# Performance work log

Measured on AMD Instinct MI355X. Metric: run time of the kernel, lower is better.

## Reference

```python
import jax, jax.numpy as jnp
import numpy as np

# Static config (from module defaults)
B, L, D, DR, R, P, PH, F = 4, 2048, 512, 256, 3, 5, 3, 1536
MAX_BANKS = 7  # S4Intelligence zero-pads unused bank slots
EPS = 1e-5


def _ln(x, s, b):
    m = x.mean(-1, keepdims=True)
    v = x.var(-1, keepdims=True)
    return (x - m) / jnp.sqrt(v + EPS) * s + b


def setup_inputs() -> dict:
    key = jax.random.key(0)
    ks = iter(jax.random.split(key, 40))
    r = lambda *s: jax.random.normal(next(ks), s, jnp.float32) * 0.02
    return dict(
        x=jax.random.normal(next(ks), (B, L, D), jnp.float32),
        reg_init=r(R, DR),
        ffn_ln_s=jnp.ones((PH, D)), ffn_ln_b=jnp.zeros((PH, D)),
        ffn_w1=r(PH, D, F), ffn_b1=jnp.zeros((PH, F)),
        ffn_w2=r(PH, F, D), ffn_b2=jnp.zeros((PH, D)),
        gate_w=r(P, PH, R * DR + D, D), gate_b=jnp.zeros((P, PH, D)),
        wproj_w=r(P, PH, R, D, DR),
        wgate_w=r(P, PH, R, D), wgate_b=jnp.zeros((P, PH, R)),
        s4_q=r(MAX_BANKS * R * DR, D), s4_k=r(D, D), s4_v=r(D, D),
        s4_sum=r(D, R * DR), s4_ln_s=jnp.ones(D), s4_ln_b=jnp.zeros(D),
        ms3_w=r(P * R * DR, P), ms3_b=jnp.zeros(P),
        m4_q=r(P * R * DR, D), m4_k=r(D, D), m4_v=r(D, D), m4_out=r(D, D),
        m4_ln_s=jnp.ones(D), m4_ln_b=jnp.zeros(D),
        out_ln_s=jnp.ones(D), out_ln_b=jnp.zeros(D),
    )


def _forward(x, reg_init, ffn_ln_s, ffn_ln_b, ffn_w1, ffn_b1, ffn_w2, ffn_b2,
             gate_w, gate_b, wproj_w, wgate_w, wgate_b,
             s4_q, s4_k, s4_v, s4_sum, s4_ln_s, s4_ln_b,
             ms3_w, ms3_b, m4_q, m4_k, m4_v, m4_out, m4_ln_s, m4_ln_b,
             out_ln_s, out_ln_b):
    scale = D ** -0.5

    # MetaS3: per-pass contribution gates from (initial) register banks
    ms3_in = jnp.tile(reg_init.reshape(-1), P)          # [P*R*DR]
    pass_w = jax.nn.sigmoid(ms3_in @ ms3_w + ms3_b)      # [P]

    def s4_read(banks, residual):
        # S4Intelligence: single-global-query attention over residual,
        # query from flattened register banks zero-padded to MAX_BANKS slots.
        flat = [bk.reshape(-1) for bk in banks]
        used = R * DR * len(banks)
        pad = MAX_BANKS * R * DR - used
        parts = flat + ([jnp.zeros((pad,), x.dtype)] if pad > 0 else [])
        q = jnp.concatenate(parts) @ s4_q                # [D]
        xn = _ln(residual, s4_ln_s, s4_ln_b)
        k = xn @ s4_k
        v = xn @ s4_v
        a = jax.nn.softmax(jnp.einsum('d,bld->bl', q, k) * scale, axis=-1)
        summ = jnp.einsum('bl,bld->bd', a, v).mean(0)    # [D]
        return (summ @ s4_sum).reshape(R, DR)            # register updates

    residual = x
    banks = []
    for p in range(P):  # 5 level-passes: L0^, L1^, L2, L1v, L0v
        regs = reg_init + s4_read(banks, residual)       # [R, DR]
        for ph in range(PH):  # prep / converge / consolidate
            xn = _ln(residual, ffn_ln_s[ph], ffn_ln_b[ph])
            delta = jax.nn.gelu(xn @ ffn_w1[ph] + ffn_b1[ph],
                                approximate=False) @ ffn_w2[ph] + ffn_b2[ph]
            # S3LevelControl.gate_phase
            summary = delta.mean((0, 1))                 # [D]
            gin = jnp.concatenate([regs.reshape(-1), summary])
            gate = jax.nn.sigmoid(gin @ gate_w[p, ph] + gate_b[p, ph])  # [D]
            residual = residual + pass_w[p] * (gate * delta)
            wg = jax.nn.sigmoid(jnp.einsum('d,rd->r', summary, wgate_w[p, ph])
                                + wgate_b[p, ph])        # [R]
            upd = jnp.einsum('d,rdk->rk', summary, wproj_w[p, ph])  # [R, DR]
            regs = regs + wg[:, None] * upd
        banks.append(regs)

    # MetaS4: final intelligence scan over all refined banks
    q = jnp.concatenate([bk.reshape(-1) for bk in banks]) @ m4_q  # [D]
    xn = _ln(residual, m4_ln_s, m4_ln_b)
    k = xn @ m4_k
    v = xn @ m4_v
    a = jax.nn.softmax(jnp.einsum('d,bld->bl', q, k) * scale, axis=-1)
    summ = jnp.einsum('bl,bld->bd', a, v)                # [B, D]
    residual = residual + (summ @ m4_out)[:, None, :]
    return _ln(residual, out_ln_s, out_ln_b)


def reference(x, reg_init, ffn_ln_s, ffn_ln_b, ffn_w1, ffn_b1, ffn_w2, ffn_b2,
              gate_w, gate_b, wproj_w, wgate_w, wgate_b,
              s4_q, s4_k, s4_v, s4_sum, s4_ln_s, s4_ln_b,
              ms3_w, ms3_b, m4_q, m4_k, m4_v, m4_out, m4_ln_s, m4_ln_b,
              out_ln_s, out_ln_b):
    return _forward(x, reg_init, ffn_ln_s, ffn_ln_b, ffn_w1, ffn_b1, ffn_w2,
                    ffn_b2, gate_w, gate_b, wproj_w, wgate_w, wgate_b,
                    s4_q, s4_k, s4_v, s4_sum, s4_ln_s, s4_ln_b,
                    ms3_w, ms3_b, m4_q, m4_k, m4_v, m4_out, m4_ln_s, m4_ln_b,
                    out_ln_s, out_ln_b)
```

## Files before the change

kernel.cpp:

```cpp
#include <hip/hip_runtime.h>
#include <stdint.h>

typedef __bf16 bf16;
typedef __bf16 bf16x8 __attribute__((ext_vector_type(8)));
typedef float floatx4 __attribute__((ext_vector_type(4)));

#define EPS 1e-5f

__device__ __forceinline__ float wave_red_sum(float v) {
#pragma unroll
  for (int off = 32; off; off >>= 1) v += __shfl_xor(v, off, 64);
  return v;
}
__device__ __forceinline__ float wave_red_max(float v) {
#pragma unroll
  for (int off = 32; off; off >>= 1) v = fmaxf(v, __shfl_xor(v, off, 64));
  return v;
}
__device__ __forceinline__ float sigmoidf(float x) { return 1.f / (1.f + expf(-x)); }

__device__ __forceinline__ void gload_lds16(const bf16* g, bf16* l) {
  __builtin_amdgcn_global_load_lds(
      (const __attribute__((address_space(1))) char*)(g),
      (__attribute__((address_space(3))) char*)(l), 16, 0, 0);
}

__global__ __launch_bounds__(256) void transpose_cast_kernel(
    const float* __restrict__ in, bf16* __restrict__ out, int R, int C) {
  __shared__ float tile[32][33];
  const size_t boff = (size_t)blockIdx.z * R * C;
  in += boff; out += boff;
  int tx = threadIdx.x, ty = threadIdx.y;
  int c0 = blockIdx.x * 32, r0 = blockIdx.y * 32;
#pragma unroll
  for (int j = 0; j < 32; j += 8)
    tile[ty + j][tx] = in[(size_t)(r0 + ty + j) * C + c0 + tx];
  __syncthreads();
#pragma unroll
  for (int j = 0; j < 32; j += 8)
    out[(size_t)(c0 + ty + j) * R + r0 + tx] = (bf16)tile[tx][ty + j];
}

template <int BM, int BN, int WM, int WN, int MODE>
__global__ __launch_bounds__(256) void gemm_kernel(
    const bf16* __restrict__ A, const bf16* __restrict__ Bt,
    const float* __restrict__ bias, bf16* __restrict__ outb,
    float* __restrict__ gsum, int N, int K) {
  constexpr int MI = WM / 16, NI = WN / 16, NWC = BN / WN;
  __shared__ bf16 As[BM * 64];
  __shared__ bf16 Bs[BN * 64];
  const int tid = threadIdx.x, l = tid & 63, w = tid >> 6;
  const int wr = w / NWC, wc = w % NWC;
  const int m0 = blockIdx.x * BM, n0 = blockIdx.y * BN;
  const int lrow8 = l >> 3;
  const int lcol8 = (((l & 7) ^ lrow8) * 8);
  const int quad = l >> 4, lane16 = l & 15;
  const int r7 = lane16 & 7;

  floatx4 acc[MI][NI];
#pragma unroll
  for (int mi = 0; mi < MI; ++mi)
#pragma unroll
    for (int ni = 0; ni < NI; ++ni) acc[mi][ni] = (floatx4){0.f, 0.f, 0.f, 0.f};

  const bf16* gA = A + (size_t)m0 * K;
  const bf16* gB = Bt + (size_t)n0 * K;

  for (int k0 = 0; k0 < K; k0 += 64) {
#pragma unroll
    for (int i = 0; i < BM / 32; ++i) {
      int rb = w * (BM / 4) + i * 8;
      gload_lds16(gA + (size_t)(rb + lrow8) * K + k0 + lcol8, As + rb * 64);
    }
#pragma unroll
    for (int i = 0; i < BN / 32; ++i) {
      int rb = w * (BN / 4) + i * 8;
      gload_lds16(gB + (size_t)(rb + lrow8) * K + k0 + lcol8, Bs + rb * 64);
    }
    __syncthreads();
#pragma unroll
    for (int kk = 0; kk < 64; kk += 32) {
      const int g = (kk >> 3) + quad;
      bf16x8 af[MI], bfv[NI];
#pragma unroll
      for (int mi = 0; mi < MI; ++mi) {
        int r = wr * WM + mi * 16 + lane16;
        af[mi] = *(const bf16x8*)(As + r * 64 + ((g ^ r7) * 8));
      }
#pragma unroll
      for (int ni = 0; ni < NI; ++ni) {
        int r = wc * WN + ni * 16 + lane16;
        bfv[ni] = *(const bf16x8*)(Bs + r * 64 + ((g ^ r7) * 8));
      }
#pragma unroll
      for (int mi = 0; mi < MI; ++mi)
#pragma unroll
        for (int ni = 0; ni < NI; ++ni)
          acc[mi][ni] = __builtin_amdgcn_mfma_f32_16x16x32_bf16(af[mi], bfv[ni], acc[mi][ni], 0, 0, 0);
    }
    __syncthreads();
  }

  float psum[NI];
#pragma unroll
  for (int ni = 0; ni < NI; ++ni) psum[ni] = 0.f;

#pragma unroll
  for (int ni = 0; ni < NI; ++ni) {
    const int gn = n0 + wc * WN + ni * 16 + lane16;
    const float bv = bias[gn];
#pragma unroll
    for (int mi = 0; mi < MI; ++mi) {
#pragma unroll
      for (int i = 0; i < 4; ++i) {
        const int gm = m0 + wr * WM + mi * 16 + quad * 4 + i;
        float v = acc[mi][ni][i] + bv;
        if constexpr (MODE == 0) {
          float ge = 0.5f * v * (1.f + erff(v * 0.7071067811865475f));
          outb[(size_t)gm * N + gn] = (bf16)ge;
        } else {
          outb[(size_t)gm * N + gn] = (bf16)v;
          psum[ni] += v;
        }
      }
    }
  }
  if constexpr (MODE == 1) {
    float* cs = (float*)As;
    __syncthreads();
    for (int t = tid; t < BN; t += 256) cs[t] = 0.f;
    __syncthreads();
#pragma unroll
    for (int ni = 0; ni < NI; ++ni)
      atomicAdd(&cs[wc * WN + ni * 16 + lane16], psum[ni]);
    __syncthreads();
    for (int t = tid; t < BN; t += 256) atomicAdd(&gsum[n0 + t], cs[t]);
  }
}

__global__ __launch_bounds__(256) void gemv_kernel(
    const float* __restrict__ vin, int vstride, const float* __restrict__ M,
    size_t mstride, int K, int N, float alpha, float* __restrict__ outp,
    int ostride) {
  const int l = threadIdx.x & 63, wv = threadIdx.x >> 6;
  const int col = blockIdx.x * 64 + l;
  const int KS = gridDim.y;
  const int Kc = (K + KS - 1) / KS;
  const int k0 = blockIdx.y * Kc;
  const int k1 = min(K, k0 + Kc);
  const float* v = vin + (size_t)blockIdx.z * vstride;
  const float* Mp = M + (size_t)blockIdx.z * mstride;
  float acc = 0.f;
  for (int k = k0 + wv; k < k1; k += 4)
    acc += v[k] * Mp[(size_t)k * N + col];
  __shared__ float sh[4][64];
  sh[wv][l] = acc;
  __syncthreads();
  if (wv == 0) {
    float r = (sh[0][l] + sh[1][l] + sh[2][l] + sh[3][l]) * alpha;
    atomicAdd(&outp[(size_t)blockIdx.z * ostride + col], r);
  }
}

__global__ __launch_bounds__(256) void small_gemvs_kernel(
    const float* __restrict__ regs, const float* __restrict__ summary,
    const float* __restrict__ gwp, const float* __restrict__ gbp,
    const float* __restrict__ wpp, float* __restrict__ gate_pre,
    float* __restrict__ ubuf) {
  const int z = blockIdx.z;
  const float* v;
  const float* M;
  float* outp;
  int K, N;
  float alpha;
  if (z == 0)      { v = regs;    M = gwp;             outp = gate_pre; K = 768; N = 512; alpha = 1.f; }
  else if (z == 1) { v = summary; M = gwp + 768 * 512; outp = gate_pre; K = 512; N = 512; alpha = 1.f / 8192.f; }
  else { int r = z - 2; v = summary; M = wpp + (size_t)r * 512 * 256; outp = ubuf + r * 256; K = 512; N = 256; alpha = 1.f / 8192.f; }
  const int l = threadIdx.x & 63, wv = threadIdx.x >> 6;
  const int col = blockIdx.x * 64 + l;
  if (blockIdx.x * 64 >= N) return;
  const int Kc = K / 8;
  const int k0 = blockIdx.y * Kc, k1 = k0 + Kc;
  float acc = 0.f;
  for (int k = k0 + wv; k < k1; k += 4)
    acc += v[k] * M[(size_t)k * N + col];
  __shared__ float sh[4][64];
  sh[wv][l] = acc;
  __syncthreads();
  if (wv == 0) {
    float r = (sh[0][l] + sh[1][l] + sh[2][l] + sh[3][l]) * alpha;
    if (z == 0 && blockIdx.y == 0) r += gbp[col];
    atomicAdd(&outp[col], r);
  }
}

__global__ __launch_bounds__(256) void init3_kernel(
    float* __restrict__ a, int na, float* __restrict__ b, int nb,
    float* __restrict__ c, const float* __restrict__ csrc, int nc) {
  const int t = blockIdx.x * 256 + threadIdx.x;
  if (t < na) a[t] = 0.f;
  if (t < nb) b[t] = 0.f;
  if (t < nc) c[t] = csrc ? csrc[t] : 0.f;
}

__global__ __launch_bounds__(256) void ln_cast_kernel(
    const float* __restrict__ res, const float* __restrict__ s,
    const float* __restrict__ b, bf16* __restrict__ xn,
    float* __restrict__ summary, float* __restrict__ gp0,
    float* __restrict__ gp1, float* __restrict__ ubuf) {
  if (blockIdx.x == 0) {
    const int t = threadIdx.x;
    summary[t] = 0.f; summary[t + 256] = 0.f;
    gp0[t] = 0.f; gp0[t + 256] = 0.f;
    gp1[t] = 0.f; gp1[t + 256] = 0.f;
    ubuf[t] = 0.f; ubuf[t + 256] = 0.f; ubuf[t + 512] = 0.f;
  }
  const int wid = threadIdx.x >> 6, l = threadIdx.x & 63;
  const int row = blockIdx.x * 4 + wid;
  const int cb = l * 8;
  const float* x = res + (size_t)row * 512 + cb;
  float4 a0 = *(const float4*)x, a1 = *(const float4*)(x + 4);
  float v[8] = {a0.x, a0.y, a0.z, a0.w, a1.x, a1.y, a1.z, a1.w};
  float sum = 0.f, sq = 0.f;
#pragma unroll
  for (int j = 0; j < 8; ++j) { sum += v[j]; sq += v[j] * v[j]; }
  sum = wave_red_sum(sum); sq = wave_red_sum(sq);
  float m = sum * (1.f / 512.f);
  float rstd = rsqrtf(sq * (1.f / 512.f) - m * m + EPS);
  bf16x8 o;
#pragma unroll
  for (int j = 0; j < 8; ++j) o[j] = (bf16)((v[j] - m) * rstd * s[cb + j] + b[cb + j]);
  *(bf16x8*)(xn + (size_t)row * 512 + cb) = o;
}

__global__ __launch_bounds__(256) void resid_ln_kernel(
    float* __restrict__ res, const bf16* __restrict__ delta,
    const float* __restrict__ gp, const float* __restrict__ passw, int p,
    const float* __restrict__ s, const float* __restrict__ b,
    bf16* __restrict__ xn) {
  const int wid = threadIdx.x >> 6, l = threadIdx.x & 63;
  const int row = blockIdx.x * 4 + wid;
  const int cb = l * 8;
  const float pw = passw[p];
  float* x = res + (size_t)row * 512 + cb;
  float4 a0 = *(const float4*)x, a1 = *(const float4*)(x + 4);
  bf16x8 dv = *(const bf16x8*)(delta + (size_t)row * 512 + cb);
  float4 g0 = *(const float4*)(gp + cb), g1 = *(const float4*)(gp + cb + 4);
  float gg[8] = {g0.x, g0.y, g0.z, g0.w, g1.x, g1.y, g1.z, g1.w};
  float v[8] = {a0.x, a0.y, a0.z, a0.w, a1.x, a1.y, a1.z, a1.w};
#pragma unroll
  for (int j = 0; j < 8; ++j) v[j] += pw * sigmoidf(gg[j]) * (float)dv[j];
  *(float4*)x = make_float4(v[0], v[1], v[2], v[3]);
  *(float4*)(x + 4) = make_float4(v[4], v[5], v[6], v[7]);
  float sum = 0.f, sq = 0.f;
#pragma unroll
  for (int j = 0; j < 8; ++j) { sum += v[j]; sq += v[j] * v[j]; }
  sum = wave_red_sum(sum); sq = wave_red_sum(sq);
  float m = sum * (1.f / 512.f);
  float rstd = rsqrtf(sq * (1.f / 512.f) - m * m + EPS);
  bf16x8 o;
#pragma unroll
  for (int j = 0; j < 8; ++j) o[j] = (bf16)((v[j] - m) * rstd * s[cb + j] + b[cb + j]);
  *(bf16x8*)(xn + (size_t)row * 512 + cb) = o;
}

__global__ __launch_bounds__(256) void attn_logits_kernel(
    const float* __restrict__ res, const float* __restrict__ s,
    const float* __restrict__ b, const float* __restrict__ kq,
    float* __restrict__ logits, float* __restrict__ czero) {
  if (blockIdx.x == 0) {
#pragma unroll
    for (int j = 0; j < 8; ++j) czero[threadIdx.x * 8 + j] = 0.f;
  }
  const int wid = threadIdx.x >> 6, l = threadIdx.x & 63;
  const int row = blockIdx.x * 4 + wid;
  const int cb = l * 8;
  const float* x = res + (size_t)row * 512 + cb;
  float4 a0 = *(const float4*)x, a1 = *(const float4*)(x + 4);
  float v[8] = {a0.x, a0.y, a0.z, a0.w, a1.x, a1.y, a1.z, a1.w};
  float sum = 0.f, sq = 0.f;
#pragma unroll
  for (int j = 0; j < 8; ++j) { sum += v[j]; sq += v[j] * v[j]; }
  sum = wave_red_sum(sum); sq = wave_red_sum(sq);
  float m = sum * (1.f / 512.f);
  float rstd = rsqrtf(sq * (1.f / 512.f) - m * m + EPS);
  float dot = 0.f;
#pragma unroll
  for (int j = 0; j < 8; ++j)
    dot += ((v[j] - m) * rstd * s[cb + j] + b[cb + j]) * kq[cb + j];
  dot = wave_red_sum(dot);
  if (l == 0) logits[row] = dot;
}

__global__ __launch_bounds__(256) void softmax_kernel(float* __restrict__ attn) {
  __shared__ float red[4];
  const int t = threadIdx.x;
  float* p = attn + blockIdx.x * 2048;
  float v[8];
#pragma unroll
  for (int j = 0; j < 8; ++j) v[j] = p[t * 8 + j];
  float mx = v[0];
#pragma unroll
  for (int j = 1; j < 8; ++j) mx = fmaxf(mx, v[j]);
  mx = wave_red_max(mx);
  if ((t & 63) == 0) red[t >> 6] = mx;
  __syncthreads();
  mx = fmaxf(fmaxf(red[0], red[1]), fmaxf(red[2], red[3]));
  __syncthreads();
  float s = 0.f;
#pragma unroll
  for (int j = 0; j < 8; ++j) { v[j] = expf(v[j] - mx); s += v[j]; }
  s = wave_red_sum(s);
  if ((t & 63) == 0) red[t >> 6] = s;
  __syncthreads();
  float inv = 1.f / (red[0] + red[1] + red[2] + red[3]);
#pragma unroll
  for (int j = 0; j < 8; ++j) p[t * 8 + j] = v[j] * inv;
}

__global__ __launch_bounds__(256) void wsum_kernel(
    const float* __restrict__ res, const float* __restrict__ s,
    const float* __restrict__ b, const float* __restrict__ attn,
    float* __restrict__ cout, int per_batch) {
  __shared__ float csh[512];
  const int tid = threadIdx.x, l = tid & 63, wv = tid >> 6;
  for (int t = tid; t < 512; t += 256) csh[t] = 0.f;
  __syncthreads();
  const int cb = l * 8;
  float sl[8], bl[8];
#pragma unroll
  for (int j = 0; j < 8; ++j) { sl[j] = s[cb + j]; bl[j] = b[cb + j]; }
  float pf[8] = {};
  const int base_row = blockIdx.x * 32;
  for (int rr = wv; rr < 32; rr += 4) {
    int row = base_row + rr;
    const float* x = res + (size_t)row * 512 + cb;
    float4 a0 = *(const float4*)x, a1 = *(const float4*)(x + 4);
    float v[8] = {a0.x, a0.y, a0.z, a0.w, a1.x, a1.y, a1.z, a1.w};
    float sum = 0.f, sq = 0.f;
#pragma unroll
    for (int j = 0; j < 8; ++j) { sum += v[j]; sq += v[j] * v[j]; }
    sum = wave_red_sum(sum); sq = wave_red_sum(sq);
    float m = sum * (1.f / 512.f);
    float rstd = rsqrtf(sq * (1.f / 512.f) - m * m + EPS);
    float aw = attn ? attn[row] : (1.f / 2048.f);
#pragma unroll
    for (int j = 0; j < 8; ++j) pf[j] += aw * ((v[j] - m) * rstd * sl[j] + bl[j]);
  }
#pragma unroll
  for (int j = 0; j < 8; ++j) atomicAdd(&csh[cb + j], pf[j]);
  __syncthreads();
  float* outp = cout + (per_batch ? (blockIdx.x >> 6) * 512 : 0);
  for (int t = tid; t < 512; t += 256) atomicAdd(&outp[t], csh[t]);
}

__global__ __launch_bounds__(256) void kq_kernel(
    const float* __restrict__ KM, const float* __restrict__ q, float scale,
    float* __restrict__ kq) {
  const int d = blockIdx.x * 4 + (threadIdx.x >> 6), l = threadIdx.x & 63;
  float a = 0.f;
  for (int j = l; j < 512; j += 64) a += KM[(size_t)d * 512 + j] * q[j];
  a = wave_red_sum(a);
  if (l == 0) kq[d] = a * scale;
}

__global__ __launch_bounds__(256) void reg_final_kernel(
    const float* __restrict__ regsA, float* __restrict__ ubuf,
    float* __restrict__ summary, const float* __restrict__ wgw,
    const float* __restrict__ wgb, float* __restrict__ regsB,
    float* __restrict__ gp_next) {
  __shared__ float wg[3];
  const int l = threadIdx.x & 63, wv = threadIdx.x >> 6;
  if (wv < 3) {
    float sg = 0.f;
    for (int d = l; d < 512; d += 64) sg += summary[d] * wgw[wv * 512 + d];
    sg = wave_red_sum(sg) * (1.f / 8192.f);
    if (l == 0) wg[wv] = sigmoidf(sg + wgb[wv]);
  }
  __syncthreads();
  for (int j = threadIdx.x; j < 768; j += 256)
    regsB[j] = regsA[j] + wg[j >> 8] * ubuf[j];
  __syncthreads();
  const int t = threadIdx.x;
  summary[t] = 0.f; summary[t + 256] = 0.f;
  gp_next[t] = 0.f; gp_next[t + 256] = 0.f;
  ubuf[t] = 0.f; ubuf[t + 256] = 0.f; ubuf[t + 512] = 0.f;
}

__global__ __launch_bounds__(64) void passw_kernel(
    const float* __restrict__ reg_init, const float* __restrict__ ms3_w,
    const float* __restrict__ ms3_b, float* __restrict__ pass_w) {
  const int l = threadIdx.x;
  float acc[5] = {};
  for (int i = l; i < 3840; i += 64) {
    float v = reg_init[i % 768];
#pragma unroll
    for (int p = 0; p < 5; ++p) acc[p] += v * ms3_w[i * 5 + p];
  }
#pragma unroll
  for (int p = 0; p < 5; ++p) acc[p] = wave_red_sum(acc[p]);
  if (l < 5) pass_w[l] = sigmoidf(acc[l] + ms3_b[l]);
}

__global__ __launch_bounds__(256) void final_out_kernel(
    const float* __restrict__ res, const float* __restrict__ outv,
    const float* __restrict__ s, const float* __restrict__ b,
    float* __restrict__ out) {
  const int wid = threadIdx.x >> 6, l = threadIdx.x & 63;
  const int row = blockIdx.x * 4 + wid;
  const int bidx = row >> 11, cb = l * 8;
  const float* x = res + (size_t)row * 512 + cb;
  const float* ov = outv + bidx * 512 + cb;
  float4 a0 = *(const float4*)x, a1 = *(const float4*)(x + 4);
  float v[8] = {a0.x, a0.y, a0.z, a0.w, a1.x, a1.y, a1.z, a1.w};
#pragma unroll
  for (int j = 0; j < 8; ++j) v[j] += ov[j];
  float sum = 0.f, sq = 0.f;
#pragma unroll
  for (int j = 0; j < 8; ++j) { sum += v[j]; sq += v[j] * v[j]; }
  sum = wave_red_sum(sum); sq = wave_red_sum(sq);
  float m = sum * (1.f / 512.f);
  float rstd = rsqrtf(sq * (1.f / 512.f) - m * m + EPS);
  float o[8];
#pragma unroll
  for (int j = 0; j < 8; ++j) o[j] = (v[j] - m) * rstd * s[cb + j] + b[cb + j];
  float* op = out + (size_t)row * 512 + cb;
  *(float4*)op = make_float4(o[0], o[1], o[2], o[3]);
  *(float4*)(op + 4) = make_float4(o[4], o[5], o[6], o[7]);
}

extern "C" void kernel_launch(void* const* d_in, const int* in_sizes, int n_in,
                              void* d_out, int out_size, void* d_ws, size_t ws_size,
                              hipStream_t stream) {
  const float* x        = (const float*)d_in[0];
  const float* reg_init = (const float*)d_in[1];
  const float* ffn_ln_s = (const float*)d_in[2];
  const float* ffn_ln_b = (const float*)d_in[3];
  const float* ffn_w1   = (const float*)d_in[4];
  const float* ffn_b1   = (const float*)d_in[5];
  const float* ffn_w2   = (const float*)d_in[6];
  const float* ffn_b2   = (const float*)d_in[7];
  const float* gate_w   = (const float*)d_in[8];
  const float* gate_b   = (const float*)d_in[9];
  const float* wproj_w  = (const float*)d_in[10];
  const float* wgate_w  = (const float*)d_in[11];
  const float* wgate_b  = (const float*)d_in[12];
  const float* s4_q     = (const float*)d_in[13];
  const float* s4_k     = (const float*)d_in[14];
  const float* s4_v     = (const float*)d_in[15];
  const float* s4_sum   = (const float*)d_in[16];
  const float* s4_ln_s  = (const float*)d_in[17];
  const float* s4_ln_b  = (const float*)d_in[18];
  const float* ms3_w    = (const float*)d_in[19];
  const float* ms3_b    = (const float*)d_in[20];
  const float* m4_q     = (const float*)d_in[21];
  const float* m4_k     = (const float*)d_in[22];
  const float* m4_v     = (const float*)d_in[23];
  const float* m4_out   = (const float*)d_in[24];
  const float* m4_ln_s  = (const float*)d_in[25];
  const float* m4_ln_b  = (const float*)d_in[26];
  const float* out_ln_s = (const float*)d_in[27];
  const float* out_ln_b = (const float*)d_in[28];
  float* out = (float*)d_out;

  char* wsp = (char*)d_ws;
  auto take = [&](size_t n) { char* p = wsp; wsp += (n + 255) & ~(size_t)255; return p; };
  float* residual = (float*)take(8192ull * 512 * 4);
  bf16*  xn       = (bf16*) take(8192ull * 512 * 2);
  bf16*  hbuf     = (bf16*) take(8192ull * 1536 * 2);
  bf16*  delta    = (bf16*) take(8192ull * 512 * 2);
  bf16*  w1t      = (bf16*) take(3ull * 1536 * 512 * 2);
  bf16*  w2t      = (bf16*) take(3ull * 512 * 1536 * 2);
  float* attn     = (float*)take(8192 * 4);
  float* cacc     = (float*)take(2048 * 4);
  float* qbuf     = (float*)take(512 * 4);
  float* kqbuf    = (float*)take(512 * 4);
  float* summary  = (float*)take(512 * 4);
  float* gp0      = (float*)take(512 * 4);
  float* gp1      = (float*)take(512 * 4);
  float* ubuf     = (float*)take(768 * 4);
  float* regsA    = (float*)take(768 * 4);
  float* regsB    = (float*)take(768 * 4);
  float* banks    = (float*)take(5 * 768 * 4);
  float* passw    = (float*)take(64);
  float* summv    = (float*)take(4 * 512 * 4);
  float* outv     = (float*)take(4 * 512 * 4);
  float* gpbuf[2] = {gp0, gp1};

  hipMemcpyAsync(residual, x, 8192ull * 512 * 4, hipMemcpyDeviceToDevice, stream);
  transpose_cast_kernel<<<dim3(1536 / 32, 512 / 32, 3), dim3(32, 8), 0, stream>>>(ffn_w1, w1t, 512, 1536);
  transpose_cast_kernel<<<dim3(512 / 32, 1536 / 32, 3), dim3(32, 8), 0, stream>>>(ffn_w2, w2t, 1536, 512);
  passw_kernel<<<1, 64, 0, stream>>>(reg_init, ms3_w, ms3_b, passw);
  ln_cast_kernel<<<2048, 256, 0, stream>>>(residual, ffn_ln_s, ffn_ln_b, xn, summary, gp0, gp1, ubuf);

  const float scale = 0.04419417382415922f;

  for (int p = 0; p < 5; ++p) {
    if (p == 0) {
      init3_kernel<<<8, 256, 0, stream>>>(cacc, 2048, summv, 512, regsA, reg_init, 768);
      wsum_kernel<<<256, 256, 0, stream>>>(residual, s4_ln_s, s4_ln_b, nullptr, cacc, 0);
    } else {
      init3_kernel<<<8, 256, 0, stream>>>(qbuf, 512, summv, 512, regsA, reg_init, 768);
      gemv_kernel<<<dim3(8, 4 * (p + 1), 1), 256, 0, stream>>>(banks, 0, s4_q, 0, p * 768, 512, 1.f, qbuf, 0);
      kq_kernel<<<128, 256, 0, stream>>>(s4_k, qbuf, scale, kqbuf);
      attn_logits_kernel<<<2048, 256, 0, stream>>>(residual, s4_ln_s, s4_ln_b, kqbuf, attn, cacc);
      softmax_kernel<<<4, 256, 0, stream>>>(attn);
      wsum_kernel<<<256, 256, 0, stream>>>(residual, s4_ln_s, s4_ln_b, attn, cacc, 0);
    }
    gemv_kernel<<<dim3(8, 8, 1), 256, 0, stream>>>(cacc, 0, s4_v, 0, 512, 512, 0.25f, summv, 0);
    gemv_kernel<<<dim3(12, 8, 1), 256, 0, stream>>>(summv, 0, s4_sum, 0, 512, 768, 1.f, regsA, 0);

    float* cur = regsA;
    float* nxt = regsB;
    for (int ph = 0; ph < 3; ++ph) {
      const int pp = p * 3 + ph;
      gemm_kernel<128, 128, 64, 64, 0><<<dim3(64, 12), 256, 0, stream>>>(
          xn, w1t + (size_t)ph * 1536 * 512, ffn_b1 + ph * 1536, hbuf, nullptr, 1536, 512);
      gemm_kernel<128, 64, 64, 32, 1><<<dim3(64, 8), 256, 0, stream>>>(
          hbuf, w2t + (size_t)ph * 512 * 1536, ffn_b2 + ph * 512, delta, summary, 512, 1536);
      small_gemvs_kernel<<<dim3(8, 8, 5), 256, 0, stream>>>(
          cur, summary, gate_w + (size_t)pp * 1280 * 512, gate_b + pp * 512,
          wproj_w + (size_t)pp * 3 * 512 * 256, gpbuf[pp & 1], ubuf);
      float* nx = (ph == 2) ? (banks + p * 768) : nxt;
      reg_final_kernel<<<1, 256, 0, stream>>>(cur, ubuf, summary, wgate_w + pp * 3 * 512,
                                              wgate_b + pp * 3, nx, gpbuf[(pp + 1) & 1]);
      const int nph = (ph + 1) % 3;
      resid_ln_kernel<<<2048, 256, 0, stream>>>(residual, delta, gpbuf[pp & 1], passw, p,
                                                ffn_ln_s + nph * 512, ffn_ln_b + nph * 512, xn);
      float* t = cur; cur = nx; nxt = (ph == 0) ? regsA : regsB; (void)t;
    }
  }

  init3_kernel<<<8, 256, 0, stream>>>(qbuf, 512, summv, 2048, outv, nullptr, 2048);
  gemv_kernel<<<dim3(8, 16, 1), 256, 0, stream>>>(banks, 0, m4_q, 0, 3840, 512, 1.f, qbuf, 0);
  kq_kernel<<<128, 256, 0, stream>>>(m4_k, qbuf, scale, kqbuf);
  attn_logits_kernel<<<2048, 256, 0, stream>>>(residual, m4_ln_s, m4_ln_b, kqbuf, attn, cacc);
  softmax_kernel<<<4, 256, 0, stream>>>(attn);
  wsum_kernel<<<256, 256, 0, stream>>>(residual, m4_ln_s, m4_ln_b, attn, cacc, 1);
  gemv_kernel<<<dim3(8, 8, 4), 256, 0, stream>>>(cacc, 512, m4_v, 0, 512, 512, 1.f, summv, 512);
  gemv_kernel<<<dim3(8, 8, 4), 256, 0, stream>>>(summv, 512, m4_out, 0, 512, 512, 1.f, outv, 512);
  final_out_kernel<<<2048, 256, 0, stream>>>(residual, outv, out_ln_s, out_ln_b, out);
}
```

Before: 1.706 ms.

## Fuse small GEMV/softmax stages with last-block tickets and cut launch count

```diff
diff --git a/kernel.cpp b/kernel.cpp
--- a/kernel.cpp
+++ b/kernel.cpp
@@ -138,89 +138,225 @@
   }
 }
 
-__global__ __launch_bounds__(256) void gemv_kernel(
+__global__ __launch_bounds__(256) void dgemv_kernel(
     const float* __restrict__ vin, int vstride, const float* __restrict__ M,
-    size_t mstride, int K, int N, float alpha, float* __restrict__ outp,
-    int ostride) {
+    size_t mstride, int K, int N, float alpha, const float* __restrict__ addv,
+    float* __restrict__ outp, int ostride) {
   const int l = threadIdx.x & 63, wv = threadIdx.x >> 6;
   const int col = blockIdx.x * 64 + l;
-  const int KS = gridDim.y;
-  const int Kc = (K + KS - 1) / KS;
-  const int k0 = blockIdx.y * Kc;
-  const int k1 = min(K, k0 + Kc);
+  const int Kc = K >> 2;
+  const int k0 = wv * Kc, k1 = k0 + Kc;
   const float* v = vin + (size_t)blockIdx.z * vstride;
   const float* Mp = M + (size_t)blockIdx.z * mstride;
   float acc = 0.f;
-  for (int k = k0 + wv; k < k1; k += 4)
-    acc += v[k] * Mp[(size_t)k * N + col];
+  for (int k = k0; k < k1; ++k) acc += v[k] * Mp[(size_t)k * N + col];
   __shared__ float sh[4][64];
   sh[wv][l] = acc;
   __syncthreads();
   if (wv == 0) {
     float r = (sh[0][l] + sh[1][l] + sh[2][l] + sh[3][l]) * alpha;
-    atomicAdd(&outp[(size_t)blockIdx.z * ostride + col], r);
-  }
-}
-
-__global__ __launch_bounds__(256) void small_gemvs_kernel(
-    const float* __restrict__ regs, const float* __restrict__ summary,
+    if (addv) r += addv[col];
+    outp[(size_t)blockIdx.z * ostride + col] = r;
+  }
+}
+
+__global__ __launch_bounds__(256) void qk_fused_kernel(
+    const float* __restrict__ banks, const float* __restrict__ s4q, int K,
+    const float* __restrict__ KM, float scale, float* __restrict__ qbuf,
+    float* __restrict__ kq, uint32_t* __restrict__ ticket) {
+  const int tid = threadIdx.x, l = tid & 63, wv = tid >> 6;
+  const int col = blockIdx.x * 64 + l;
+  const int Kc = K >> 2;
+  float acc = 0.f;
+  for (int k = wv * Kc; k < (wv + 1) * Kc; ++k) acc += banks[k] * s4q[(size_t)k * 512 + col];
+  __shared__ float sh[4][64];
+  sh[wv][l] = acc;
+  __syncthreads();
+  if (wv == 0) qbuf[col] = sh[0][l] + sh[1][l] + sh[2][l] + sh[3][l];
+  __threadfence();
+  __shared__ uint32_t lastv;
+  if (tid == 0) lastv = atomicAdd(ticket, 1u);
+  __syncthreads();
+  if (lastv != gridDim.x - 1) return;
+  __threadfence();
+  __shared__ float qs[512];
+  qs[tid] = qbuf[tid]; qs[tid + 256] = qbuf[tid + 256];
+  __syncthreads();
+  for (int i = tid; i < 512; i += 256) {
+    const float* row = KM + (size_t)i * 512;
+    float a = 0.f;
+#pragma unroll 4
+    for (int j = 0; j < 512; ++j) a += row[j] * qs[j];
+    kq[i] = a * scale;
+  }
+  if (tid == 0) atomicExch(ticket, 0u);
+}
+
+__global__ __launch_bounds__(256) void attn_ls_kernel(
+    const float* __restrict__ res, const float* __restrict__ s,
+    const float* __restrict__ b, const float* __restrict__ kq,
+    float* __restrict__ logits, float* __restrict__ stats,
+    float* __restrict__ cacc, uint32_t* __restrict__ ticket) {
+  const int tid = threadIdx.x, wid = tid >> 6, l = tid & 63;
+  const int cb = l * 8;
+#pragma unroll
+  for (int rr = 0; rr < 2; ++rr) {
+    const int row = blockIdx.x * 8 + rr * 4 + wid;
+    const float* x = res + (size_t)row * 512 + cb;
+    float4 a0 = *(const float4*)x, a1 = *(const float4*)(x + 4);
+    float v[8] = {a0.x, a0.y, a0.z, a0.w, a1.x, a1.y, a1.z, a1.w};
+    float sum = 0.f, sq = 0.f;
+#pragma unroll
+    for (int j = 0; j < 8; ++j) { sum += v[j]; sq += v[j] * v[j]; }
+    sum = wave_red_sum(sum); sq = wave_red_sum(sq);
+    float m = sum * (1.f / 512.f);
+    float rstd = rsqrtf(sq * (1.f / 512.f) - m * m + EPS);
+    float dot = 0.f;
+#pragma unroll
+    for (int j = 0; j < 8; ++j)
+      dot += ((v[j] - m) * rstd * s[cb + j] + b[cb + j]) * kq[cb + j];
+    dot = wave_red_sum(dot);
+    if (l == 0) logits[row] = dot;
+  }
+  __threadfence();
+  __shared__ uint32_t lastv;
+  if (tid == 0) lastv = atomicAdd(ticket, 1u);
+  __syncthreads();
+  if (lastv != gridDim.x - 1) return;
+  __threadfence();
+  float vv[32];
+  const float* lp = logits + wid * 2048;
+  float mx = -1e30f;
+#pragma unroll
+  for (int i = 0; i < 32; ++i) { vv[i] = lp[l + 64 * i]; mx = fmaxf(mx, vv[i]); }
+  mx = wave_red_max(mx);
+  float sum = 0.f;
+#pragma unroll
+  for (int i = 0; i < 32; ++i) sum += expf(vv[i] - mx);
+  sum = wave_red_sum(sum);
+  if (l == 0) { stats[wid] = mx; stats[4 + wid] = 1.f / sum; }
+  for (int t = tid; t < 2048; t += 256) cacc[t] = 0.f;
+  if (tid == 0) atomicExch(ticket, 0u);
+}
+
+__global__ __launch_bounds__(256) void wsum_kernel(
+    const float* __restrict__ res, const float* __restrict__ s,
+    const float* __restrict__ b, const float* __restrict__ logits,
+    const float* __restrict__ stats, float* __restrict__ cout, int per_batch) {
+  __shared__ float csh[512];
+  const int tid = threadIdx.x, l = tid & 63, wv = tid >> 6;
+  for (int t = tid; t < 512; t += 256) csh[t] = 0.f;
+  __syncthreads();
+  const int cb = l * 8;
+  float sl[8], bl[8];
+#pragma unroll
+  for (int j = 0; j < 8; ++j) { sl[j] = s[cb + j]; bl[j] = b[cb + j]; }
+  float pf[8] = {};
+  const int base_row = blockIdx.x * 32;
+  for (int rr = wv; rr < 32; rr += 4) {
+    int row = base_row + rr;
+    const float* x = res + (size_t)row * 512 + cb;
+    float4 a0 = *(const float4*)x, a1 = *(const float4*)(x + 4);
+    float v[8] = {a0.x, a0.y, a0.z, a0.w, a1.x, a1.y, a1.z, a1.w};
+    float sum = 0.f, sq = 0.f;
+#pragma unroll
+    for (int j = 0; j < 8; ++j) { sum += v[j]; sq += v[j] * v[j]; }
+    sum = wave_red_sum(sum); sq = wave_red_sum(sq);
+    float m = sum * (1.f / 512.f);
+    float rstd = rsqrtf(sq * (1.f / 512.f) - m * m + EPS);
+    float aw;
+    if (logits) {
+      int bb = row >> 11;
+      aw = expf(logits[row] - stats[bb]) * stats[4 + bb];
+    } else {
+      aw = 1.f / 2048.f;
+    }
+#pragma unroll
+    for (int j = 0; j < 8; ++j) pf[j] += aw * ((v[j] - m) * rstd * sl[j] + bl[j]);
+  }
+#pragma unroll
+  for (int j = 0; j < 8; ++j) atomicAdd(&csh[cb + j], pf[j]);
+  __syncthreads();
+  float* outp = cout + (per_batch ? (blockIdx.x >> 6) * 512 : 0);
+  for (int t = tid; t < 512; t += 256) atomicAdd(&outp[t], csh[t]);
+}
+
+__global__ __launch_bounds__(256) void small_fused_kernel(
+    const float* __restrict__ regs, float* __restrict__ summary,
     const float* __restrict__ gwp, const float* __restrict__ gbp,
     const float* __restrict__ wpp, float* __restrict__ gate_pre,
-    float* __restrict__ ubuf) {
+    float* __restrict__ ubuf, const float* __restrict__ wgw,
+    const float* __restrict__ wgb, float* __restrict__ regsB,
+    float* __restrict__ gp_next, uint32_t* __restrict__ ticket) {
+  const int tid = threadIdx.x, l = tid & 63, wv = tid >> 6;
   const int z = blockIdx.z;
-  const float* v;
-  const float* M;
-  float* outp;
-  int K, N;
-  float alpha;
-  if (z == 0)      { v = regs;    M = gwp;             outp = gate_pre; K = 768; N = 512; alpha = 1.f; }
-  else if (z == 1) { v = summary; M = gwp + 768 * 512; outp = gate_pre; K = 512; N = 512; alpha = 1.f / 8192.f; }
-  else { int r = z - 2; v = summary; M = wpp + (size_t)r * 512 * 256; outp = ubuf + r * 256; K = 512; N = 256; alpha = 1.f / 8192.f; }
-  const int l = threadIdx.x & 63, wv = threadIdx.x >> 6;
-  const int col = blockIdx.x * 64 + l;
-  if (blockIdx.x * 64 >= N) return;
-  const int Kc = K / 8;
-  const int k0 = blockIdx.y * Kc, k1 = k0 + Kc;
-  float acc = 0.f;
-  for (int k = k0 + wv; k < k1; k += 4)
-    acc += v[k] * M[(size_t)k * N + col];
-  __shared__ float sh[4][64];
-  sh[wv][l] = acc;
-  __syncthreads();
-  if (wv == 0) {
-    float r = (sh[0][l] + sh[1][l] + sh[2][l] + sh[3][l]) * alpha;
-    if (z == 0 && blockIdx.y == 0) r += gbp[col];
-    atomicAdd(&outp[col], r);
-  }
-}
-
-__global__ __launch_bounds__(256) void init3_kernel(
-    float* __restrict__ a, int na, float* __restrict__ b, int nb,
-    float* __restrict__ c, const float* __restrict__ csrc, int nc) {
-  const int t = blockIdx.x * 256 + threadIdx.x;
-  if (t < na) a[t] = 0.f;
-  if (t < nb) b[t] = 0.f;
-  if (t < nc) c[t] = csrc ? csrc[t] : 0.f;
-}
-
-__global__ __launch_bounds__(256) void ln_cast_kernel(
-    const float* __restrict__ res, const float* __restrict__ s,
-    const float* __restrict__ b, bf16* __restrict__ xn,
-    float* __restrict__ summary, float* __restrict__ gp0,
-    float* __restrict__ gp1, float* __restrict__ ubuf) {
+  if (!(z >= 2 && blockIdx.x >= 4)) {
+    const float* v;
+    const float* M;
+    float* outp;
+    int K; float alpha;
+    if (z == 0)      { v = regs;    M = gwp;             outp = gate_pre; K = 768; alpha = 1.f; }
+    else if (z == 1) { v = summary; M = gwp + 768 * 512; outp = gate_pre; K = 512; alpha = 1.f / 8192.f; }
+    else { int r = z - 2; v = summary; M = wpp + (size_t)r * 512 * 256; outp = ubuf + r * 256; K = 512; alpha = 1.f / 8192.f; }
+    const int N = (z < 2) ? 512 : 256;
+    const int col = blockIdx.x * 64 + l;
+    const int Kc = K >> 3;
+    const int k0 = blockIdx.y * Kc, k1 = k0 + Kc;
+    float acc = 0.f;
+    for (int k = k0 + wv; k < k1; k += 4) acc += v[k] * M[(size_t)k * N + col];
+    __shared__ float sh[4][64];
+    sh[wv][l] = acc;
+    __syncthreads();
+    if (wv == 0) {
+      float r = (sh[0][l] + sh[1][l] + sh[2][l] + sh[3][l]) * alpha;
+      if (z == 0 && blockIdx.y == 0) r += gbp[col];
+      atomicAdd(&outp[col], r);
+    }
+  }
+  __threadfence();
+  __shared__ uint32_t lastv;
+  if (tid == 0) lastv = atomicAdd(ticket, 1u);
+  __syncthreads();
+  if (lastv != 320 - 1) return;
+  __threadfence();
+  __shared__ float wg[3];
+  if (wv < 3) {
+    float sg = 0.f;
+    for (int d = l; d < 512; d += 64) sg += summary[d] * wgw[wv * 512 + d];
+    sg = wave_red_sum(sg) * (1.f / 8192.f);
+    if (l == 0) wg[wv] = sigmoidf(sg + wgb[wv]);
+  }
+  __syncthreads();
+  for (int j = tid; j < 768; j += 256) regsB[j] = regs[j] + wg[j >> 8] * ubuf[j];
+  __syncthreads();
+  summary[tid] = 0.f; summary[tid + 256] = 0.f;
+  gp_next[tid] = 0.f; gp_next[tid + 256] = 0.f;
+  ubuf[tid] = 0.f; ubuf[tid + 256] = 0.f; ubuf[tid + 512] = 0.f;
+  if (tid == 0) atomicExch(ticket, 0u);
+}
+
+__global__ __launch_bounds__(256) void ln_cast_first_kernel(
+    const float* __restrict__ x, const float* __restrict__ s,
+    const float* __restrict__ b, float* __restrict__ residual,
+    bf16* __restrict__ xn, float* __restrict__ summary, float* __restrict__ gp0,
+    float* __restrict__ gp1, float* __restrict__ ubuf, float* __restrict__ cacc) {
   if (blockIdx.x == 0) {
     const int t = threadIdx.x;
     summary[t] = 0.f; summary[t + 256] = 0.f;
     gp0[t] = 0.f; gp0[t + 256] = 0.f;
     gp1[t] = 0.f; gp1[t + 256] = 0.f;
     ubuf[t] = 0.f; ubuf[t + 256] = 0.f; ubuf[t + 512] = 0.f;
+#pragma unroll
+    for (int j = 0; j < 8; ++j) cacc[t * 8 + j] = 0.f;
   }
   const int wid = threadIdx.x >> 6, l = threadIdx.x & 63;
   const int row = blockIdx.x * 4 + wid;
   const int cb = l * 8;
-  const float* x = res + (size_t)row * 512 + cb;
-  float4 a0 = *(const float4*)x, a1 = *(const float4*)(x + 4);
+  const float* xp = x + (size_t)row * 512 + cb;
+  float4 a0 = *(const float4*)xp, a1 = *(const float4*)(xp + 4);
   float v[8] = {a0.x, a0.y, a0.z, a0.w, a1.x, a1.y, a1.z, a1.w};
+  float* rp = residual + (size_t)row * 512 + cb;
+  *(float4*)rp = a0; *(float4*)(rp + 4) = a1;
   float sum = 0.f, sq = 0.f;
 #pragma unroll
   for (int j = 0; j < 8; ++j) { sum += v[j]; sq += v[j] * v[j]; }
@@ -264,133 +400,12 @@
   *(bf16x8*)(xn + (size_t)row * 512 + cb) = o;
 }
 
-__global__ __launch_bounds__(256) void attn_logits_kernel(
-    const float* __restrict__ res, const float* __restrict__ s,
-    const float* __restrict__ b, const float* __restrict__ kq,
-    float* __restrict__ logits, float* __restrict__ czero) {
-  if (blockIdx.x == 0) {
-#pragma unroll
-    for (int j = 0; j < 8; ++j) czero[threadIdx.x * 8 + j] = 0.f;
-  }
-  const int wid = threadIdx.x >> 6, l = threadIdx.x & 63;
-  const int row = blockIdx.x * 4 + wid;
-  const int cb = l * 8;
-  const float* x = res + (size_t)row * 512 + cb;
-  float4 a0 = *(const float4*)x, a1 = *(const float4*)(x + 4);
-  float v[8] = {a0.x, a0.y, a0.z, a0.w, a1.x, a1.y, a1.z, a1.w};
-  float sum = 0.f, sq = 0.f;
-#pragma unroll
-  for (int j = 0; j < 8; ++j) { sum += v[j]; sq += v[j] * v[j]; }
-  sum = wave_red_sum(sum); sq = wave_red_sum(sq);
-  float m = sum * (1.f / 512.f);
-  float rstd = rsqrtf(sq * (1.f / 512.f) - m * m + EPS);
-  float dot = 0.f;
-#pragma unroll
-  for (int j = 0; j < 8; ++j)
-    dot += ((v[j] - m) * rstd * s[cb + j] + b[cb + j]) * kq[cb + j];
-  dot = wave_red_sum(dot);
-  if (l == 0) logits[row] = dot;
-}
-
-__global__ __launch_bounds__(256) void softmax_kernel(float* __restrict__ attn) {
-  __shared__ float red[4];
-  const int t = threadIdx.x;
-  float* p = attn + blockIdx.x * 2048;
-  float v[8];
-#pragma unroll
-  for (int j = 0; j < 8; ++j) v[j] = p[t * 8 + j];
-  float mx = v[0];
-#pragma unroll
-  for (int j = 1; j < 8; ++j) mx = fmaxf(mx, v[j]);
-  mx = wave_red_max(mx);
-  if ((t & 63) == 0) red[t >> 6] = mx;
-  __syncthreads();
-  mx = fmaxf(fmaxf(red[0], red[1]), fmaxf(red[2], red[3]));
-  __syncthreads();
-  float s = 0.f;
-#pragma unroll
-  for (int j = 0; j < 8; ++j) { v[j] = expf(v[j] - mx); s += v[j]; }
-  s = wave_red_sum(s);
-  if ((t & 63) == 0) red[t >> 6] = s;
-  __syncthreads();
-  float inv = 1.f / (red[0] + red[1] + red[2] + red[3]);
-#pragma unroll
-  for (int j = 0; j < 8; ++j) p[t * 8 + j] = v[j] * inv;
-}
-
-__global__ __launch_bounds__(256) void wsum_kernel(
-    const float* __restrict__ res, const float* __restrict__ s,
-    const float* __restrict__ b, const float* __restrict__ attn,
-    float* __restrict__ cout, int per_batch) {
-  __shared__ float csh[512];
-  const int tid = threadIdx.x, l = tid & 63, wv = tid >> 6;
-  for (int t = tid; t < 512; t += 256) csh[t] = 0.f;
-  __syncthreads();
-  const int cb = l * 8;
-  float sl[8], bl[8];
-#pragma unroll
-  for (int j = 0; j < 8; ++j) { sl[j] = s[cb + j]; bl[j] = b[cb + j]; }
-  float pf[8] = {};
-  const int base_row = blockIdx.x * 32;
-  for (int rr = wv; rr < 32; rr += 4) {
-    int row = base_row + rr;
-    const float* x = res + (size_t)row * 512 + cb;
-    float4 a0 = *(const float4*)x, a1 = *(const float4*)(x + 4);
-    float v[8] = {a0.x, a0.y, a0.z, a0.w, a1.x, a1.y, a1.z, a1.w};
-    float sum = 0.f, sq = 0.f;
-#pragma unroll
-    for (int j = 0; j < 8; ++j) { sum += v[j]; sq += v[j] * v[j]; }
-    sum = wave_red_sum(sum); sq = wave_red_sum(sq);
-    float m = sum * (1.f / 512.f);
-    float rstd = rsqrtf(sq * (1.f / 512.f) - m * m + EPS);
-    float aw = attn ? attn[row] : (1.f / 2048.f);
-#pragma unroll
-    for (int j = 0; j < 8; ++j) pf[j] += aw * ((v[j] - m) * rstd * sl[j] + bl[j]);
-  }
-#pragma unroll
-  for (int j = 0; j < 8; ++j) atomicAdd(&csh[cb + j], pf[j]);
-  __syncthreads();
-  float* outp = cout + (per_batch ? (blockIdx.x >> 6) * 512 : 0);
-  for (int t = tid; t < 512; t += 256) atomicAdd(&outp[t], csh[t]);
-}
-
-__global__ __launch_bounds__(256) void kq_kernel(
-    const float* __restrict__ KM, const float* __restrict__ q, float scale,
-    float* __restrict__ kq) {
-  const int d = blockIdx.x * 4 + (threadIdx.x >> 6), l = threadIdx.x & 63;
-  float a = 0.f;
-  for (int j = l; j < 512; j += 64) a += KM[(size_t)d * 512 + j] * q[j];
-  a = wave_red_sum(a);
-  if (l == 0) kq[d] = a * scale;
-}
-
-__global__ __launch_bounds__(256) void reg_final_kernel(
-    const float* __restrict__ regsA, float* __restrict__ ubuf,
-    float* __restrict__ summary, const float* __restrict__ wgw,
-    const float* __restrict__ wgb, float* __restrict__ regsB,
-    float* __restrict__ gp_next) {
-  __shared__ float wg[3];
-  const int l = threadIdx.x & 63, wv = threadIdx.x >> 6;
-  if (wv < 3) {
-    float sg = 0.f;
-    for (int d = l; d < 512; d += 64) sg += summary[d] * wgw[wv * 512 + d];
-    sg = wave_red_sum(sg) * (1.f / 8192.f);
-    if (l == 0) wg[wv] = sigmoidf(sg + wgb[wv]);
-  }
-  __syncthreads();
-  for (int j = threadIdx.x; j < 768; j += 256)
-    regsB[j] = regsA[j] + wg[j >> 8] * ubuf[j];
-  __syncthreads();
-  const int t = threadIdx.x;
-  summary[t] = 0.f; summary[t + 256] = 0.f;
-  gp_next[t] = 0.f; gp_next[t + 256] = 0.f;
-  ubuf[t] = 0.f; ubuf[t + 256] = 0.f; ubuf[t + 512] = 0.f;
-}
-
 __global__ __launch_bounds__(64) void passw_kernel(
     const float* __restrict__ reg_init, const float* __restrict__ ms3_w,
-    const float* __restrict__ ms3_b, float* __restrict__ pass_w) {
+    const float* __restrict__ ms3_b, float* __restrict__ pass_w,
+    uint32_t* __restrict__ tickets) {
   const int l = threadIdx.x;
+  if (l < 16) tickets[l] = 0u;
   float acc[5] = {};
   for (int i = l; i < 3840; i += 64) {
     float v = reg_init[i % 768];
@@ -471,7 +486,8 @@
   bf16*  delta    = (bf16*) take(8192ull * 512 * 2);
   bf16*  w1t      = (bf16*) take(3ull * 1536 * 512 * 2);
   bf16*  w2t      = (bf16*) take(3ull * 512 * 1536 * 2);
-  float* attn     = (float*)take(8192 * 4);
+  float* logits   = (float*)take(8192 * 4);
+  float* stats    = (float*)take(8 * 4);
   float* cacc     = (float*)take(2048 * 4);
   float* qbuf     = (float*)take(512 * 4);
   float* kqbuf    = (float*)take(512 * 4);
@@ -485,30 +501,27 @@
   float* passw    = (float*)take(64);
   float* summv    = (float*)take(4 * 512 * 4);
   float* outv     = (float*)take(4 * 512 * 4);
+  uint32_t* tickets = (uint32_t*)take(64 * 4);
   float* gpbuf[2] = {gp0, gp1};
 
-  hipMemcpyAsync(residual, x, 8192ull * 512 * 4, hipMemcpyDeviceToDevice, stream);
   transpose_cast_kernel<<<dim3(1536 / 32, 512 / 32, 3), dim3(32, 8), 0, stream>>>(ffn_w1, w1t, 512, 1536);
   transpose_cast_kernel<<<dim3(512 / 32, 1536 / 32, 3), dim3(32, 8), 0, stream>>>(ffn_w2, w2t, 1536, 512);
-  passw_kernel<<<1, 64, 0, stream>>>(reg_init, ms3_w, ms3_b, passw);
-  ln_cast_kernel<<<2048, 256, 0, stream>>>(residual, ffn_ln_s, ffn_ln_b, xn, summary, gp0, gp1, ubuf);
+  passw_kernel<<<1, 64, 0, stream>>>(reg_init, ms3_w, ms3_b, passw, tickets);
+  ln_cast_first_kernel<<<2048, 256, 0, stream>>>(x, ffn_ln_s, ffn_ln_b, residual, xn,
+                                                 summary, gp0, gp1, ubuf, cacc);
 
   const float scale = 0.04419417382415922f;
 
   for (int p = 0; p < 5; ++p) {
-    if (p == 0) {
-      init3_kernel<<<8, 256, 0, stream>>>(cacc, 2048, summv, 512, regsA, reg_init, 768);
-      wsum_kernel<<<256, 256, 0, stream>>>(residual, s4_ln_s, s4_ln_b, nullptr, cacc, 0);
+    if (p > 0) {
+      qk_fused_kernel<<<8, 256, 0, stream>>>(banks, s4_q, p * 768, s4_k, scale, qbuf, kqbuf, &tickets[0]);
+      attn_ls_kernel<<<256, 256, 0, stream>>>(residual, s4_ln_s, s4_ln_b, kqbuf, logits, stats, cacc, &tickets[1]);
+      wsum_kernel<<<256, 256, 0, stream>>>(residual, s4_ln_s, s4_ln_b, logits, stats, cacc, 0);
     } else {
-      init3_kernel<<<8, 256, 0, stream>>>(qbuf, 512, summv, 512, regsA, reg_init, 768);
-      gemv_kernel<<<dim3(8, 4 * (p + 1), 1), 256, 0, stream>>>(banks, 0, s4_q, 0, p * 768, 512, 1.f, qbuf, 0);
-      kq_kernel<<<128, 256, 0, stream>>>(s4_k, qbuf, scale, kqbuf);
-      attn_logits_kernel<<<2048, 256, 0, stream>>>(residual, s4_ln_s, s4_ln_b, kqbuf, attn, cacc);
-      softmax_kernel<<<4, 256, 0, stream>>>(attn);
-      wsum_kernel<<<256, 256, 0, stream>>>(residual, s4_ln_s, s4_ln_b, attn, cacc, 0);
-    }
-    gemv_kernel<<<dim3(8, 8, 1), 256, 0, stream>>>(cacc, 0, s4_v, 0, 512, 512, 0.25f, summv, 0);
-    gemv_kernel<<<dim3(12, 8, 1), 256, 0, stream>>>(summv, 0, s4_sum, 0, 512, 768, 1.f, regsA, 0);
+      wsum_kernel<<<256, 256, 0, stream>>>(residual, s4_ln_s, s4_ln_b, nullptr, nullptr, cacc, 0);
+    }
+    dgemv_kernel<<<dim3(8, 1, 1), 256, 0, stream>>>(cacc, 0, s4_v, 0, 512, 512, 0.25f, nullptr, summv, 0);
+    dgemv_kernel<<<dim3(12, 1, 1), 256, 0, stream>>>(summv, 0, s4_sum, 0, 512, 768, 1.f, reg_init, regsA, 0);
 
     float* cur = regsA;
     float* nxt = regsB;
@@ -518,12 +531,11 @@
           xn, w1t + (size_t)ph * 1536 * 512, ffn_b1 + ph * 1536, hbuf, nullptr, 1536, 512);
       gemm_kernel<128, 64, 64, 32, 1><<<dim3(64, 8), 256, 0, stream>>>(
           hbuf, w2t + (size_t)ph * 512 * 1536, ffn_b2 + ph * 512, delta, summary, 512, 1536);
-      small_gemvs_kernel<<<dim3(8, 8, 5), 256, 0, stream>>>(
+      float* nx = (ph == 2) ? (banks + p * 768) : nxt;
+      small_fused_kernel<<<dim3(8, 8, 5), 256, 0, stream>>>(
           cur, summary, gate_w + (size_t)pp * 1280 * 512, gate_b + pp * 512,
-          wproj_w + (size_t)pp * 3 * 512 * 256, gpbuf[pp & 1], ubuf);
-      float* nx = (ph == 2) ? (banks + p * 768) : nxt;
-      reg_final_kernel<<<1, 256, 0, stream>>>(cur, ubuf, summary, wgate_w + pp * 3 * 512,
-                                              wgate_b + pp * 3, nx, gpbuf[(pp + 1) & 1]);
+          wproj_w + (size_t)pp * 3 * 512 * 256, gpbuf[pp & 1], ubuf,
+          wgate_w + pp * 3 * 512, wgate_b + pp * 3, nx, gpbuf[(pp + 1) & 1], &tickets[2]);
       const int nph = (ph + 1) % 3;
       resid_ln_kernel<<<2048, 256, 0, stream>>>(residual, delta, gpbuf[pp & 1], passw, p,
                                                 ffn_ln_s + nph * 512, ffn_ln_b + nph * 512, xn);
@@ -531,13 +543,10 @@
     }
   }
 
-  init3_kernel<<<8, 256, 0, stream>>>(qbuf, 512, summv, 2048, outv, nullptr, 2048);
-  gemv_kernel<<<dim3(8, 16, 1), 256, 0, stream>>>(banks, 0, m4_q, 0, 3840, 512, 1.f, qbuf, 0);
-  kq_kernel<<<128, 256, 0, stream>>>(m4_k, qbuf, scale, kqbuf);
-  attn_logits_kernel<<<2048, 256, 0, stream>>>(residual, m4_ln_s, m4_ln_b, kqbuf, attn, cacc);
-  softmax_kernel<<<4, 256, 0, stream>>>(attn);
-  wsum_kernel<<<256, 256, 0, stream>>>(residual, m4_ln_s, m4_ln_b, attn, cacc, 1);
-  gemv_kernel<<<dim3(8, 8, 4), 256, 0, stream>>>(cacc, 512, m4_v, 0, 512, 512, 1.f, summv, 512);
-  gemv_kernel<<<dim3(8, 8, 4), 256, 0, stream>>>(summv, 512, m4_out, 0, 512, 512, 1.f, outv, 512);
+  qk_fused_kernel<<<8, 256, 0, stream>>>(banks, m4_q, 3840, m4_k, scale, qbuf, kqbuf, &tickets[0]);
+  attn_ls_kernel<<<256, 256, 0, stream>>>(residual, m4_ln_s, m4_ln_b, kqbuf, logits, stats, cacc, &tickets[1]);
+  wsum_kernel<<<256, 256, 0, stream>>>(residual, m4_ln_s, m4_ln_b, logits, stats, cacc, 1);
+  dgemv_kernel<<<dim3(8, 1, 4), 256, 0, stream>>>(cacc, 512, m4_v, 0, 512, 512, 1.f, nullptr, summv, 512);
+  dgemv_kernel<<<dim3(8, 1, 4), 256, 0, stream>>>(summv, 512, m4_out, 0, 512, 512, 1.f, nullptr, outv, 512);
   final_out_kernel<<<2048, 256, 0, stream>>>(residual, outv, out_ln_s, out_ln_b, out);
 }
```

Result: slower. 3.717 ms (+117.9%).
